# Kernel optimization log

Hardware: AMD Instinct MI355X
Metric: run time of the kernel (lower is better)

## Reference

```python
import jax, jax.numpy as jnp
import numpy as np

N_NODES = 100000
N_EDGES = 1600000
IN_FEAT = 128
OUT_FEAT = 64
RRELU_SLOPE = (1.0 / 8.0 + 1.0 / 3.0) / 2.0  # nn.RReLU eval-mode slope = 11/48


def setup_inputs() -> dict:
    key = jax.random.key(0)
    k1, k2, k3, k4, k5 = jax.random.split(key, 5)
    feat = jax.random.normal(k1, (N_NODES, IN_FEAT), dtype=jnp.float32)
    src = jax.random.randint(k2, (N_EDGES,), 0, N_NODES, dtype=jnp.int64)
    dst = jax.random.randint(k3, (N_EDGES,), 0, N_NODES, dtype=jnp.int64)
    # xavier-uniform-ish init
    b1 = np.sqrt(6.0 / (IN_FEAT + OUT_FEAT))
    b2 = np.sqrt(6.0 / (OUT_FEAT + OUT_FEAT))
    w1 = jax.random.uniform(k4, (IN_FEAT, OUT_FEAT), jnp.float32, -b1, b1)
    w2 = jax.random.uniform(k5, (OUT_FEAT, OUT_FEAT), jnp.float32, -b2, b2)
    return {"feat": feat, "src": src, "dst": dst, "w1": w1, "w2": w2}


def _gather_sum(h, src, dst):
    # DGL copy_src('h','m') + sum: for each dst node, sum messages from src nodes
    return jax.ops.segment_sum(h[src], dst, num_segments=N_NODES)


def _rrelu(x):
    return jnp.where(x >= 0, x, RRELU_SLOPE * x)


def reference(feat, src, dst, w1, w2):
    # pattern = 0: linear -> gather -> rrelu, linear -> gather -> rrelu
    h = feat @ w1                      # [N, out_feat]
    h = _gather_sum(h, src, dst)       # [N, out_feat]
    h = _rrelu(h)
    h = h @ w2                         # [N, out_feat]
    h = _gather_sum(h, src, dst)       # [N, out_feat]
    h = _rrelu(h)
    return h
```

## Files before the change

kernel.cpp:

```cpp
#include <hip/hip_runtime.h>

#define N_NODES 100000
#define N_EDGES 1600000
#define IN_FEAT 128
#define OUT_FEAT 64
#define SLOPE 0.22916666666666666f

#define NPB 128
#define NB 782
#define CAP 2560
#define BIN_CHUNK 8192
#define EPT 32
#define BIN_BLOCKS ((N_EDGES + BIN_CHUNK - 1) / BIN_CHUNK)
#define GEMM1_BLOCKS (N_NODES / 16)

__device__ __forceinline__ ushort f2bf(float x) {
    unsigned u = __float_as_uint(x);
    u += 0x7FFFu + ((u >> 16) & 1u);
    return (ushort)(u >> 16);
}

union FatSmem {
    struct { float f[16 * IN_FEAT]; float part[4 * 16 * OUT_FEAT]; } g;
    struct { int cnt[NB]; int gbase[NB]; } b;
};

__global__ __launch_bounds__(256) void gemm1_binning_kernel(
        const float* __restrict__ feat, const float* __restrict__ w1,
        ushort* __restrict__ h1,
        const int* __restrict__ src, const int* __restrict__ dst,
        int* __restrict__ bcur, int* __restrict__ pairs) {
    __shared__ FatSmem s;
    const int tid = threadIdx.x;

    if (blockIdx.x >= BIN_BLOCKS) {
        const int c = tid & 63;
        const int ks = tid >> 6;

        float wr[32];
#pragma unroll
        for (int j = 0; j < 32; ++j)
            wr[j] = w1[(ks * 32 + j) * OUT_FEAT + c];

        const int row0 = (blockIdx.x - BIN_BLOCKS) * 16;
        const float4* fg = (const float4*)(feat + (size_t)row0 * IN_FEAT);
        float4* fl = (float4*)s.g.f;
        fl[tid] = fg[tid];
        fl[tid + 256] = fg[tid + 256];
        __syncthreads();

        float acc[16];
#pragma unroll
        for (int r = 0; r < 16; ++r) acc[r] = 0.f;

        const float4* fv = (const float4*)s.g.f;
#pragma unroll
        for (int j4 = 0; j4 < 8; ++j4) {
            const float wa = wr[4 * j4], wb = wr[4 * j4 + 1];
            const float wc = wr[4 * j4 + 2], wd = wr[4 * j4 + 3];
#pragma unroll
            for (int r = 0; r < 16; ++r) {
                const float4 a = fv[r * 32 + ks * 8 + j4];
                acc[r] += a.x * wa + a.y * wb + a.z * wc + a.w * wd;
            }
        }

#pragma unroll
        for (int r = 0; r < 16; ++r)
            s.g.part[ks * (16 * OUT_FEAT) + r * OUT_FEAT + c] = acc[r];
        __syncthreads();

        ushort2* h1u2 = (ushort2*)h1;
#pragma unroll
        for (int half = 0; half < 2; ++half) {
            const int idx = half * 256 + tid;
            const int r = idx >> 5;
            const int cp = idx & 31;
            const float* p = s.g.part + r * OUT_FEAT + 2 * cp;
            const float lo = p[0] + p[1024] + p[2048] + p[3072];
            const float hi = p[1] + p[1025] + p[2049] + p[3073];
            h1u2[(size_t)(row0 + r) * 32 + cp] = make_ushort2(f2bf(lo), f2bf(hi));
        }
    } else {
        int* cnt = s.b.cnt;
        int* gbase = s.b.gbase;
        for (int i = tid; i < NB; i += 256) cnt[i] = 0;
        __syncthreads();
        const int base = blockIdx.x * BIN_CHUNK;
        int bl[EPT];
        int vp[EPT];
#pragma unroll
        for (int i = 0; i < EPT; ++i) {
            const int e = base + i * 256 + tid;
            if (e < N_EDGES) {
                const int d = dst[e];
                const int b = d >> 7;
                const int lpos = atomicAdd(&cnt[b], 1);
                bl[i] = (b << 13) | lpos;
                vp[i] = ((d & 127) << 17) | src[e];
            } else {
                bl[i] = -1;
            }
        }
        __syncthreads();
        for (int i = tid; i < NB; i += 256) {
            const int cc = cnt[i];
            gbase[i] = cc ? (i * CAP + atomicAdd(&bcur[i], cc)) : 0;
        }
        __syncthreads();
#pragma unroll
        for (int i = 0; i < EPT; ++i) {
            if (bl[i] >= 0) {
                const int b = bl[i] >> 13, lpos = bl[i] & 8191;
                pairs[gbase[b] + lpos] = vp[i];
            }
        }
    }
}

__global__ __launch_bounds__(256) void sort2_kernel(const int* __restrict__ pairs,
                                                    const int* __restrict__ bcur,
                                                    int* __restrict__ csr,
                                                    int2* __restrict__ nseg) {
    __shared__ int cnt[NPB];
    __shared__ int cur[NPB];
    __shared__ int wtot;
    const int b = blockIdx.x;
    const int t = threadIdx.x;
    const int beg = b * CAP;
    const int end = beg + bcur[b];
    if (t < NPB) cnt[t] = 0;
    __syncthreads();
    for (int i = beg + t; i < end; i += 256)
        atomicAdd(&cnt[pairs[i] >> 17], 1);
    __syncthreads();
    int v = 0, x = 0;
    const int lane = t & 63, w = t >> 6;
    if (t < NPB) {
        v = cnt[t];
        x = v;
#pragma unroll
        for (int off = 1; off < 64; off <<= 1) {
            int y = __shfl_up(x, off);
            if (lane >= off) x += y;
        }
        if (t == 63) wtot = x;
    }
    __syncthreads();
    if (t < NPB) {
        const int gp = beg + (x - v) + (w ? wtot : 0);
        cur[t] = gp;
        nseg[b * NPB + t] = make_int2(gp, gp + v);
    }
    __syncthreads();
    for (int i = beg + t; i < end; i += 256) {
        const int p = pairs[i];
        const int pos = atomicAdd(&cur[p >> 17], 1);
        csr[pos] = (p & 0x1FFFF) << 7;
    }
}

__device__ __forceinline__ float2 gather_pairs(const char* __restrict__ hb,
                                               const int* __restrict__ csr,
                                               int beg, int end, int hi, int cp4) {
    float ax = 0.f, ay = 0.f;
    int i = beg;
#define LOADU(k) const unsigned u##k = *(const unsigned*)(hb + (unsigned)(csr[i + 2*(k) + hi] + cp4))
#define ACCU(k)                                            \
    ax += __uint_as_float(u##k << 16);                     \
    ay += __uint_as_float(u##k & 0xFFFF0000u)
    for (; i + 16 <= end; i += 16) {
        LOADU(0); LOADU(1); LOADU(2); LOADU(3);
        LOADU(4); LOADU(5); LOADU(6); LOADU(7);
        ACCU(0); ACCU(1); ACCU(2); ACCU(3);
        ACCU(4); ACCU(5); ACCU(6); ACCU(7);
    }
    if (i + 8 <= end) {
        LOADU(0); LOADU(1); LOADU(2); LOADU(3);
        ACCU(0); ACCU(1); ACCU(2); ACCU(3);
        i += 8;
    }
    if (i + 4 <= end) {
        LOADU(0); LOADU(1);
        ACCU(0); ACCU(1);
        i += 4;
    }
    for (; i < end; i += 2) {
        if (i + hi < end) {
            const unsigned u = *(const unsigned*)(hb + (unsigned)(csr[i + hi] + cp4));
            ax += __uint_as_float(u << 16);
            ay += __uint_as_float(u & 0xFFFF0000u);
        }
    }
#undef LOADU
#undef ACCU
    return make_float2(ax, ay);
}

__global__ __launch_bounds__(256) void agg_gemm2_kernel(const ushort* __restrict__ h,
                                                        const int* __restrict__ csr,
                                                        const int2* __restrict__ nseg,
                                                        const float* __restrict__ w2,
                                                        ushort* __restrict__ h2) {
    __shared__ float w[OUT_FEAT * OUT_FEAT];
    __shared__ float rowbuf[4][OUT_FEAT];
    const int tid = threadIdx.x;

    const float4* w4g = (const float4*)w2;
    float4* wl = (float4*)w;
#pragma unroll
    for (int i = 0; i < 4; ++i) wl[tid + i * 256] = w4g[tid + i * 256];
    __syncthreads();

    const int wv = tid >> 6, c = tid & 63;
    const int hi = (tid >> 5) & 1, cp = tid & 31;
    const int node = blockIdx.x * 4 + wv;
    const int2 seg = nseg[node];
    const int beg = __builtin_amdgcn_readfirstlane(seg.x);
    const int end = __builtin_amdgcn_readfirstlane(seg.y);

    float2 acc = gather_pairs((const char*)h, csr, beg, end, hi, cp * 4);
    acc.x += __shfl_xor(acc.x, 32);
    acc.y += __shfl_xor(acc.y, 32);
    acc.x = acc.x >= 0.f ? acc.x : acc.x * SLOPE;
    acc.y = acc.y >= 0.f ? acc.y : acc.y * SLOPE;

    if (hi == 0) ((float2*)rowbuf[wv])[cp] = acc;

    float o = 0.f;
    const float4* rb4 = (const float4*)rowbuf[wv];
#pragma unroll
    for (int k = 0; k < OUT_FEAT; k += 4) {
        const float4 r = rb4[k >> 2];
        o += r.x * w[(k + 0) * OUT_FEAT + c] + r.y * w[(k + 1) * OUT_FEAT + c] +
             r.z * w[(k + 2) * OUT_FEAT + c] + r.w * w[(k + 3) * OUT_FEAT + c];
    }
    h2[(size_t)node * OUT_FEAT + c] = f2bf(o);
}

__global__ __launch_bounds__(256) void agg_rrelu_kernel(const ushort* __restrict__ h,
                                                        const int* __restrict__ csr,
                                                        const int2* __restrict__ nseg,
                                                        float* __restrict__ out) {
    const int tid = threadIdx.x;
    const int hi = (tid >> 5) & 1, cp = tid & 31;
    const int node = blockIdx.x * 4 + (tid >> 6);
    const int2 seg = nseg[node];
    const int beg = __builtin_amdgcn_readfirstlane(seg.x);
    const int end = __builtin_amdgcn_readfirstlane(seg.y);

    float2 acc = gather_pairs((const char*)h, csr, beg, end, hi, cp * 4);
    acc.x += __shfl_xor(acc.x, 32);
    acc.y += __shfl_xor(acc.y, 32);
    if (hi == 0) {
        acc.x = acc.x >= 0.f ? acc.x : acc.x * SLOPE;
        acc.y = acc.y >= 0.f ? acc.y : acc.y * SLOPE;
        ((float2*)(out + (size_t)node * OUT_FEAT))[cp] = acc;
    }
}

extern "C" void kernel_launch(void* const* d_in, const int* in_sizes, int n_in,
                              void* d_out, int out_size, void* d_ws, size_t ws_size,
                              hipStream_t stream) {
    const float* feat = (const float*)d_in[0];
    const int*   src  = (const int*)d_in[1];
    const int*   dst  = (const int*)d_in[2];
    const float* w1   = (const float*)d_in[3];
    const float* w2   = (const float*)d_in[4];
    float* out = (float*)d_out;

    ushort* h1   = (ushort*)d_ws;
    ushort* h2   = h1 + (size_t)N_NODES * OUT_FEAT;
    int*    pairs = (int*)h2;
    int*    csr  = (int*)(h2 + (size_t)N_NODES * OUT_FEAT);
    int2*   nseg = (int2*)(csr + NB * CAP);
    int*    bcur = (int*)(nseg + NB * NPB);

    hipMemsetAsync(bcur, 0, NB * sizeof(int), stream);
    gemm1_binning_kernel<<<BIN_BLOCKS + GEMM1_BLOCKS, 256, 0, stream>>>(
        feat, w1, h1, src, dst, bcur, pairs);
    sort2_kernel<<<NB, 256, 0, stream>>>(pairs, bcur, csr, nseg);

    agg_gemm2_kernel<<<N_NODES / 4, 256, 0, stream>>>(h1, csr, nseg, w2, h2);

    agg_rrelu_kernel<<<N_NODES / 4, 256, 0, stream>>>(h2, csr, nseg, out);
}
```

Baseline: 167.5 us.

## Widen gather to 8-byte quad loads and co-schedule GEMM1 with sort pass

The neighbor gather now has each 16-lane group load 4 bf16 features (8 bytes) per edge, processing 4 edges concurrently per wave. Edge indices are fetched with one coalesced csr read and broadcast by shuffles, followed by a cross-group reduction. Separately, the first GEMM moves from the binning launch to the sort launch, so binning runs alone and GEMM1 overlaps the per-bin counting sort. This aims to cut the number of gather memory instructions and rebalance work between launches, at the cost of extra shuffles and a reduction at the end.

```diff
diff --git a/kernel.cpp b/kernel.cpp
--- a/kernel.cpp
+++ b/kernel.cpp
@@ -20,20 +20,59 @@
     return (ushort)(u >> 16);
 }
 
-union FatSmem {
+__global__ __launch_bounds__(256) void binning_kernel(const int* __restrict__ src,
+                                                      const int* __restrict__ dst,
+                                                      int* __restrict__ bcur,
+                                                      int* __restrict__ pairs) {
+    __shared__ int cnt[NB];
+    __shared__ int gbase[NB];
+    for (int i = threadIdx.x; i < NB; i += 256) cnt[i] = 0;
+    __syncthreads();
+    const int base = blockIdx.x * BIN_CHUNK;
+    int bl[EPT];
+    int vp[EPT];
+#pragma unroll
+    for (int i = 0; i < EPT; ++i) {
+        const int e = base + i * 256 + threadIdx.x;
+        if (e < N_EDGES) {
+            const int d = dst[e];
+            const int b = d >> 7;
+            const int lpos = atomicAdd(&cnt[b], 1);
+            bl[i] = (b << 13) | lpos;
+            vp[i] = ((d & 127) << 17) | src[e];
+        } else {
+            bl[i] = -1;
+        }
+    }
+    __syncthreads();
+    for (int i = threadIdx.x; i < NB; i += 256) {
+        const int c = cnt[i];
+        gbase[i] = c ? (i * CAP + atomicAdd(&bcur[i], c)) : 0;
+    }
+    __syncthreads();
+#pragma unroll
+    for (int i = 0; i < EPT; ++i) {
+        if (bl[i] >= 0) {
+            const int b = bl[i] >> 13, lpos = bl[i] & 8191;
+            pairs[gbase[b] + lpos] = vp[i];
+        }
+    }
+}
+
+union Fat2Smem {
     struct { float f[16 * IN_FEAT]; float part[4 * 16 * OUT_FEAT]; } g;
-    struct { int cnt[NB]; int gbase[NB]; } b;
+    struct { int cnt[NPB]; int cur[NPB]; int wtot; } s;
 };
 
-__global__ __launch_bounds__(256) void gemm1_binning_kernel(
+__global__ __launch_bounds__(256) void sort2_gemm1_kernel(
+        const int* __restrict__ pairs, const int* __restrict__ bcur,
+        int* __restrict__ csr, int2* __restrict__ nseg,
         const float* __restrict__ feat, const float* __restrict__ w1,
-        ushort* __restrict__ h1,
-        const int* __restrict__ src, const int* __restrict__ dst,
-        int* __restrict__ bcur, int* __restrict__ pairs) {
-    __shared__ FatSmem s;
+        ushort* __restrict__ h1) {
+    __shared__ Fat2Smem u;
     const int tid = threadIdx.x;
 
-    if (blockIdx.x >= BIN_BLOCKS) {
+    if (blockIdx.x >= NB) {
         const int c = tid & 63;
         const int ks = tid >> 6;
 
@@ -42,9 +81,9 @@
         for (int j = 0; j < 32; ++j)
             wr[j] = w1[(ks * 32 + j) * OUT_FEAT + c];
 
-        const int row0 = (blockIdx.x - BIN_BLOCKS) * 16;
+        const int row0 = (blockIdx.x - NB) * 16;
         const float4* fg = (const float4*)(feat + (size_t)row0 * IN_FEAT);
-        float4* fl = (float4*)s.g.f;
+        float4* fl = (float4*)u.g.f;
         fl[tid] = fg[tid];
         fl[tid + 256] = fg[tid + 256];
         __syncthreads();
@@ -53,7 +92,7 @@
 #pragma unroll
         for (int r = 0; r < 16; ++r) acc[r] = 0.f;
 
-        const float4* fv = (const float4*)s.g.f;
+        const float4* fv = (const float4*)u.g.f;
 #pragma unroll
         for (int j4 = 0; j4 < 8; ++j4) {
             const float wa = wr[4 * j4], wb = wr[4 * j4 + 1];
@@ -67,7 +106,7 @@
 
 #pragma unroll
         for (int r = 0; r < 16; ++r)
-            s.g.part[ks * (16 * OUT_FEAT) + r * OUT_FEAT + c] = acc[r];
+            u.g.part[ks * (16 * OUT_FEAT) + r * OUT_FEAT + c] = acc[r];
         __syncthreads();
 
         ushort2* h1u2 = (ushort2*)h1;
@@ -76,125 +115,97 @@
             const int idx = half * 256 + tid;
             const int r = idx >> 5;
             const int cp = idx & 31;
-            const float* p = s.g.part + r * OUT_FEAT + 2 * cp;
+            const float* p = u.g.part + r * OUT_FEAT + 2 * cp;
             const float lo = p[0] + p[1024] + p[2048] + p[3072];
             const float hi = p[1] + p[1025] + p[2049] + p[3073];
             h1u2[(size_t)(row0 + r) * 32 + cp] = make_ushort2(f2bf(lo), f2bf(hi));
         }
     } else {
-        int* cnt = s.b.cnt;
-        int* gbase = s.b.gbase;
-        for (int i = tid; i < NB; i += 256) cnt[i] = 0;
-        __syncthreads();
-        const int base = blockIdx.x * BIN_CHUNK;
-        int bl[EPT];
-        int vp[EPT];
-#pragma unroll
-        for (int i = 0; i < EPT; ++i) {
-            const int e = base + i * 256 + tid;
-            if (e < N_EDGES) {
-                const int d = dst[e];
-                const int b = d >> 7;
-                const int lpos = atomicAdd(&cnt[b], 1);
-                bl[i] = (b << 13) | lpos;
-                vp[i] = ((d & 127) << 17) | src[e];
-            } else {
-                bl[i] = -1;
+        const int b = blockIdx.x;
+        const int beg = b * CAP;
+        const int end = beg + bcur[b];
+        if (tid < NPB) u.s.cnt[tid] = 0;
+        __syncthreads();
+        for (int i = beg + tid; i < end; i += 256)
+            atomicAdd(&u.s.cnt[pairs[i] >> 17], 1);
+        __syncthreads();
+        int v = 0, x = 0;
+        const int lane = tid & 63, w = tid >> 6;
+        if (tid < NPB) {
+            v = u.s.cnt[tid];
+            x = v;
+#pragma unroll
+            for (int off = 1; off < 64; off <<= 1) {
+                int y = __shfl_up(x, off);
+                if (lane >= off) x += y;
             }
-        }
-        __syncthreads();
-        for (int i = tid; i < NB; i += 256) {
-            const int cc = cnt[i];
-            gbase[i] = cc ? (i * CAP + atomicAdd(&bcur[i], cc)) : 0;
-        }
-        __syncthreads();
-#pragma unroll
-        for (int i = 0; i < EPT; ++i) {
-            if (bl[i] >= 0) {
-                const int b = bl[i] >> 13, lpos = bl[i] & 8191;
-                pairs[gbase[b] + lpos] = vp[i];
-            }
-        }
-    }
-}
-
-__global__ __launch_bounds__(256) void sort2_kernel(const int* __restrict__ pairs,
-                                                    const int* __restrict__ bcur,
-                                                    int* __restrict__ csr,
-                                                    int2* __restrict__ nseg) {
-    __shared__ int cnt[NPB];
-    __shared__ int cur[NPB];
-    __shared__ int wtot;
-    const int b = blockIdx.x;
-    const int t = threadIdx.x;
-    const int beg = b * CAP;
-    const int end = beg + bcur[b];
-    if (t < NPB) cnt[t] = 0;
-    __syncthreads();
-    for (int i = beg + t; i < end; i += 256)
-        atomicAdd(&cnt[pairs[i] >> 17], 1);
-    __syncthreads();
-    int v = 0, x = 0;
-    const int lane = t & 63, w = t >> 6;
-    if (t < NPB) {
-        v = cnt[t];
-        x = v;
-#pragma unroll
-        for (int off = 1; off < 64; off <<= 1) {
-            int y = __shfl_up(x, off);
-            if (lane >= off) x += y;
-        }
-        if (t == 63) wtot = x;
-    }
-    __syncthreads();
-    if (t < NPB) {
-        const int gp = beg + (x - v) + (w ? wtot : 0);
-        cur[t] = gp;
-        nseg[b * NPB + t] = make_int2(gp, gp + v);
-    }
-    __syncthreads();
-    for (int i = beg + t; i < end; i += 256) {
-        const int p = pairs[i];
-        const int pos = atomicAdd(&cur[p >> 17], 1);
-        csr[pos] = (p & 0x1FFFF) << 7;
-    }
-}
-
-__device__ __forceinline__ float2 gather_pairs(const char* __restrict__ hb,
-                                               const int* __restrict__ csr,
-                                               int beg, int end, int hi, int cp4) {
-    float ax = 0.f, ay = 0.f;
+            if (tid == 63) u.s.wtot = x;
+        }
+        __syncthreads();
+        if (tid < NPB) {
+            const int gp = beg + (x - v) + (w ? u.s.wtot : 0);
+            u.s.cur[tid] = gp;
+            nseg[b * NPB + tid] = make_int2(gp, gp + v);
+        }
+        __syncthreads();
+        for (int i = beg + tid; i < end; i += 256) {
+            const int p = pairs[i];
+            const int pos = atomicAdd(&u.s.cur[p >> 17], 1);
+            csr[pos] = (p & 0x1FFFF) << 7;
+        }
+    }
+}
+
+__device__ __forceinline__ float4 gather_quad(const char* __restrict__ hb,
+                                              const int* __restrict__ csr,
+                                              int beg, int end, int lane) {
+    const int g = (lane >> 4) & 3;
+    const unsigned q8 = (unsigned)((lane & 15) * 8);
+    float ax = 0.f, ay = 0.f, az = 0.f, aw = 0.f;
     int i = beg;
-#define LOADU(k) const unsigned u##k = *(const unsigned*)(hb + (unsigned)(csr[i + 2*(k) + hi] + cp4))
-#define ACCU(k)                                            \
-    ax += __uint_as_float(u##k << 16);                     \
-    ay += __uint_as_float(u##k & 0xFFFF0000u)
+#define QACC(u)                                   \
+    ax += __uint_as_float((u).x << 16);           \
+    ay += __uint_as_float((u).x & 0xFFFF0000u);   \
+    az += __uint_as_float((u).y << 16);           \
+    aw += __uint_as_float((u).y & 0xFFFF0000u)
     for (; i + 16 <= end; i += 16) {
-        LOADU(0); LOADU(1); LOADU(2); LOADU(3);
-        LOADU(4); LOADU(5); LOADU(6); LOADU(7);
-        ACCU(0); ACCU(1); ACCU(2); ACCU(3);
-        ACCU(4); ACCU(5); ACCU(6); ACCU(7);
-    }
-    if (i + 8 <= end) {
-        LOADU(0); LOADU(1); LOADU(2); LOADU(3);
-        ACCU(0); ACCU(1); ACCU(2); ACCU(3);
-        i += 8;
-    }
-    if (i + 4 <= end) {
-        LOADU(0); LOADU(1);
-        ACCU(0); ACCU(1);
-        i += 4;
-    }
-    for (; i < end; i += 2) {
-        if (i + hi < end) {
-            const unsigned u = *(const unsigned*)(hb + (unsigned)(csr[i + hi] + cp4));
-            ax += __uint_as_float(u << 16);
-            ay += __uint_as_float(u & 0xFFFF0000u);
-        }
-    }
-#undef LOADU
-#undef ACCU
-    return make_float2(ax, ay);
+        const int csv = csr[i + (lane & 15)];
+        const int r0 = __shfl(csv, g);
+        const int r1 = __shfl(csv, 4 + g);
+        const int r2 = __shfl(csv, 8 + g);
+        const int r3 = __shfl(csv, 12 + g);
+        const uint2 u0 = *(const uint2*)(hb + ((unsigned)r0 + q8));
+        const uint2 u1 = *(const uint2*)(hb + ((unsigned)r1 + q8));
+        const uint2 u2 = *(const uint2*)(hb + ((unsigned)r2 + q8));
+        const uint2 u3 = *(const uint2*)(hb + ((unsigned)r3 + q8));
+        QACC(u0); QACC(u1); QACC(u2); QACC(u3);
+    }
+    for (; i + 4 <= end; i += 4) {
+        const int c0 = csr[i], c1 = csr[i + 1], c2 = csr[i + 2], c3 = csr[i + 3];
+        const int r = g == 0 ? c0 : (g == 1 ? c1 : (g == 2 ? c2 : c3));
+        const uint2 u = *(const uint2*)(hb + ((unsigned)r + q8));
+        QACC(u);
+    }
+    if (i < end) {
+        const int rem = end - i;
+        const int r = csr[i + (g < rem ? g : 0)];
+        const uint2 u = *(const uint2*)(hb + ((unsigned)r + q8));
+        if (g < rem) { QACC(u); }
+    }
+#undef QACC
+    ax += __shfl_xor(ax, 16); ax += __shfl_xor(ax, 32);
+    ay += __shfl_xor(ay, 16); ay += __shfl_xor(ay, 32);
+    az += __shfl_xor(az, 16); az += __shfl_xor(az, 32);
+    aw += __shfl_xor(aw, 16); aw += __shfl_xor(aw, 32);
+    return make_float4(ax, ay, az, aw);
+}
+
+__device__ __forceinline__ float4 rrelu4(float4 v) {
+    v.x = v.x >= 0.f ? v.x : v.x * SLOPE;
+    v.y = v.y >= 0.f ? v.y : v.y * SLOPE;
+    v.z = v.z >= 0.f ? v.z : v.z * SLOPE;
+    v.w = v.w >= 0.f ? v.w : v.w * SLOPE;
+    return v;
 }
 
 __global__ __launch_bounds__(256) void agg_gemm2_kernel(const ushort* __restrict__ h,
@@ -212,20 +223,16 @@
     for (int i = 0; i < 4; ++i) wl[tid + i * 256] = w4g[tid + i * 256];
     __syncthreads();
 
-    const int wv = tid >> 6, c = tid & 63;
-    const int hi = (tid >> 5) & 1, cp = tid & 31;
+    const int wv = tid >> 6, lane = tid & 63, c = tid & 63;
     const int node = blockIdx.x * 4 + wv;
     const int2 seg = nseg[node];
     const int beg = __builtin_amdgcn_readfirstlane(seg.x);
     const int end = __builtin_amdgcn_readfirstlane(seg.y);
 
-    float2 acc = gather_pairs((const char*)h, csr, beg, end, hi, cp * 4);
-    acc.x += __shfl_xor(acc.x, 32);
-    acc.y += __shfl_xor(acc.y, 32);
-    acc.x = acc.x >= 0.f ? acc.x : acc.x * SLOPE;
-    acc.y = acc.y >= 0.f ? acc.y : acc.y * SLOPE;
-
-    if (hi == 0) ((float2*)rowbuf[wv])[cp] = acc;
+    float4 a = gather_quad((const char*)h, csr, beg, end, lane);
+    a = rrelu4(a);
+
+    if ((lane >> 4) == 0) ((float4*)rowbuf[wv])[lane & 15] = a;
 
     float o = 0.f;
     const float4* rb4 = (const float4*)rowbuf[wv];
@@ -243,19 +250,16 @@
                                                         const int2* __restrict__ nseg,
                                                         float* __restrict__ out) {
     const int tid = threadIdx.x;
-    const int hi = (tid >> 5) & 1, cp = tid & 31;
+    const int lane = tid & 63;
     const int node = blockIdx.x * 4 + (tid >> 6);
     const int2 seg = nseg[node];
     const int beg = __builtin_amdgcn_readfirstlane(seg.x);
     const int end = __builtin_amdgcn_readfirstlane(seg.y);
 
-    float2 acc = gather_pairs((const char*)h, csr, beg, end, hi, cp * 4);
-    acc.x += __shfl_xor(acc.x, 32);
-    acc.y += __shfl_xor(acc.y, 32);
-    if (hi == 0) {
-        acc.x = acc.x >= 0.f ? acc.x : acc.x * SLOPE;
-        acc.y = acc.y >= 0.f ? acc.y : acc.y * SLOPE;
-        ((float2*)(out + (size_t)node * OUT_FEAT))[cp] = acc;
+    float4 a = gather_quad((const char*)h, csr, beg, end, lane);
+    if ((lane >> 4) == 0) {
+        a = rrelu4(a);
+        ((float4*)(out + (size_t)node * OUT_FEAT))[lane & 15] = a;
     }
 }
 
@@ -277,9 +281,9 @@
     int*    bcur = (int*)(nseg + NB * NPB);
 
     hipMemsetAsync(bcur, 0, NB * sizeof(int), stream);
-    gemm1_binning_kernel<<<BIN_BLOCKS + GEMM1_BLOCKS, 256, 0, stream>>>(
-        feat, w1, h1, src, dst, bcur, pairs);
-    sort2_kernel<<<NB, 256, 0, stream>>>(pairs, bcur, csr, nseg);
+    binning_kernel<<<BIN_BLOCKS, 256, 0, stream>>>(src, dst, bcur, pairs);
+    sort2_gemm1_kernel<<<NB + GEMM1_BLOCKS, 256, 0, stream>>>(
+        pairs, bcur, csr, nseg, feat, w1, h1);
 
     agg_gemm2_kernel<<<N_NODES / 4, 256, 0, stream>>>(h1, csr, nseg, w2, h2);
 
```

After: 189.8 us (median of 2 runs). 1.13x slower.

## Pair gemm1 with sort stage instead of binning; transpose w2 in LDS

Applied to the files above, without the earlier changes.

Moves the feature GEMM blocks out of the binning launch and into the per-bucket sort launch, so the binning kernel runs alone and the sort work overlaps with the GEMM instead. In the aggregate+GEMM2 kernel, w2 is stored transposed in shared memory with padded rows, so each thread reads contiguous float4 weights rather than strided scalars. The rebalanced kernel split may change how well memory-bound binning and compute-bound GEMM overlap. The transposed store adds a strided global read of w2 per block.

```diff
diff --git a/kernel.cpp b/kernel.cpp
--- a/kernel.cpp
+++ b/kernel.cpp
@@ -13,6 +13,7 @@
 #define EPT 32
 #define BIN_BLOCKS ((N_EDGES + BIN_CHUNK - 1) / BIN_CHUNK)
 #define GEMM1_BLOCKS (N_NODES / 16)
+#define WTS 68
 
 __device__ __forceinline__ ushort f2bf(float x) {
     unsigned u = __float_as_uint(x);
@@ -20,20 +21,59 @@
     return (ushort)(u >> 16);
 }
 
-union FatSmem {
+__global__ __launch_bounds__(256) void binning_kernel(const int* __restrict__ src,
+                                                      const int* __restrict__ dst,
+                                                      int* __restrict__ bcur,
+                                                      int* __restrict__ pairs) {
+    __shared__ int cnt[NB];
+    __shared__ int gbase[NB];
+    for (int i = threadIdx.x; i < NB; i += 256) cnt[i] = 0;
+    __syncthreads();
+    const int base = blockIdx.x * BIN_CHUNK;
+    int bl[EPT];
+    int vp[EPT];
+#pragma unroll
+    for (int i = 0; i < EPT; ++i) {
+        const int e = base + i * 256 + threadIdx.x;
+        if (e < N_EDGES) {
+            const int d = dst[e];
+            const int b = d >> 7;
+            const int lpos = atomicAdd(&cnt[b], 1);
+            bl[i] = (b << 13) | lpos;
+            vp[i] = ((d & 127) << 17) | src[e];
+        } else {
+            bl[i] = -1;
+        }
+    }
+    __syncthreads();
+    for (int i = threadIdx.x; i < NB; i += 256) {
+        const int c = cnt[i];
+        gbase[i] = c ? (i * CAP + atomicAdd(&bcur[i], c)) : 0;
+    }
+    __syncthreads();
+#pragma unroll
+    for (int i = 0; i < EPT; ++i) {
+        if (bl[i] >= 0) {
+            const int b = bl[i] >> 13, lpos = bl[i] & 8191;
+            pairs[gbase[b] + lpos] = vp[i];
+        }
+    }
+}
+
+union Fat2Smem {
     struct { float f[16 * IN_FEAT]; float part[4 * 16 * OUT_FEAT]; } g;
-    struct { int cnt[NB]; int gbase[NB]; } b;
+    struct { int cnt[NPB]; int cur[NPB]; int wtot; } s;
 };
 
-__global__ __launch_bounds__(256) void gemm1_binning_kernel(
+__global__ __launch_bounds__(256) void sort2_gemm1_kernel(
+        const int* __restrict__ pairs, const int* __restrict__ bcur,
+        int* __restrict__ csr, int2* __restrict__ nseg,
         const float* __restrict__ feat, const float* __restrict__ w1,
-        ushort* __restrict__ h1,
-        const int* __restrict__ src, const int* __restrict__ dst,
-        int* __restrict__ bcur, int* __restrict__ pairs) {
-    __shared__ FatSmem s;
+        ushort* __restrict__ h1) {
+    __shared__ Fat2Smem u;
     const int tid = threadIdx.x;
 
-    if (blockIdx.x >= BIN_BLOCKS) {
+    if (blockIdx.x >= NB) {
         const int c = tid & 63;
         const int ks = tid >> 6;
 
@@ -42,9 +82,9 @@
         for (int j = 0; j < 32; ++j)
             wr[j] = w1[(ks * 32 + j) * OUT_FEAT + c];
 
-        const int row0 = (blockIdx.x - BIN_BLOCKS) * 16;
+        const int row0 = (blockIdx.x - NB) * 16;
         const float4* fg = (const float4*)(feat + (size_t)row0 * IN_FEAT);
-        float4* fl = (float4*)s.g.f;
+        float4* fl = (float4*)u.g.f;
         fl[tid] = fg[tid];
         fl[tid + 256] = fg[tid + 256];
         __syncthreads();
@@ -53,7 +93,7 @@
 #pragma unroll
         for (int r = 0; r < 16; ++r) acc[r] = 0.f;
 
-        const float4* fv = (const float4*)s.g.f;
+        const float4* fv = (const float4*)u.g.f;
 #pragma unroll
         for (int j4 = 0; j4 < 8; ++j4) {
             const float wa = wr[4 * j4], wb = wr[4 * j4 + 1];
@@ -67,7 +107,7 @@
 
 #pragma unroll
         for (int r = 0; r < 16; ++r)
-            s.g.part[ks * (16 * OUT_FEAT) + r * OUT_FEAT + c] = acc[r];
+            u.g.part[ks * (16 * OUT_FEAT) + r * OUT_FEAT + c] = acc[r];
         __syncthreads();
 
         ushort2* h1u2 = (ushort2*)h1;
@@ -76,87 +116,44 @@
             const int idx = half * 256 + tid;
             const int r = idx >> 5;
             const int cp = idx & 31;
-            const float* p = s.g.part + r * OUT_FEAT + 2 * cp;
+            const float* p = u.g.part + r * OUT_FEAT + 2 * cp;
             const float lo = p[0] + p[1024] + p[2048] + p[3072];
             const float hi = p[1] + p[1025] + p[2049] + p[3073];
             h1u2[(size_t)(row0 + r) * 32 + cp] = make_ushort2(f2bf(lo), f2bf(hi));
         }
     } else {
-        int* cnt = s.b.cnt;
-        int* gbase = s.b.gbase;
-        for (int i = tid; i < NB; i += 256) cnt[i] = 0;
-        __syncthreads();
-        const int base = blockIdx.x * BIN_CHUNK;
-        int bl[EPT];
-        int vp[EPT];
-#pragma unroll
-        for (int i = 0; i < EPT; ++i) {
-            const int e = base + i * 256 + tid;
-            if (e < N_EDGES) {
-                const int d = dst[e];
-                const int b = d >> 7;
-                const int lpos = atomicAdd(&cnt[b], 1);
-                bl[i] = (b << 13) | lpos;
-                vp[i] = ((d & 127) << 17) | src[e];
-            } else {
-                bl[i] = -1;
+        const int b = blockIdx.x;
+        const int beg = b * CAP;
+        const int end = beg + bcur[b];
+        if (tid < NPB) u.s.cnt[tid] = 0;
+        __syncthreads();
+        for (int i = beg + tid; i < end; i += 256)
+            atomicAdd(&u.s.cnt[pairs[i] >> 17], 1);
+        __syncthreads();
+        int v = 0, x = 0;
+        const int lane = tid & 63, w = tid >> 6;
+        if (tid < NPB) {
+            v = u.s.cnt[tid];
+            x = v;
+#pragma unroll
+            for (int off = 1; off < 64; off <<= 1) {
+                int y = __shfl_up(x, off);
+                if (lane >= off) x += y;
             }
-        }
-        __syncthreads();
-        for (int i = tid; i < NB; i += 256) {
-            const int cc = cnt[i];
-            gbase[i] = cc ? (i * CAP + atomicAdd(&bcur[i], cc)) : 0;
-        }
-        __syncthreads();
-#pragma unroll
-        for (int i = 0; i < EPT; ++i) {
-            if (bl[i] >= 0) {
-                const int b = bl[i] >> 13, lpos = bl[i] & 8191;
-                pairs[gbase[b] + lpos] = vp[i];
-            }
-        }
-    }
-}
-
-__global__ __launch_bounds__(256) void sort2_kernel(const int* __restrict__ pairs,
-                                                    const int* __restrict__ bcur,
-                                                    int* __restrict__ csr,
-                                                    int2* __restrict__ nseg) {
-    __shared__ int cnt[NPB];
-    __shared__ int cur[NPB];
-    __shared__ int wtot;
-    const int b = blockIdx.x;
-    const int t = threadIdx.x;
-    const int beg = b * CAP;
-    const int end = beg + bcur[b];
-    if (t < NPB) cnt[t] = 0;
-    __syncthreads();
-    for (int i = beg + t; i < end; i += 256)
-        atomicAdd(&cnt[pairs[i] >> 17], 1);
-    __syncthreads();
-    int v = 0, x = 0;
-    const int lane = t & 63, w = t >> 6;
-    if (t < NPB) {
-        v = cnt[t];
-        x = v;
-#pragma unroll
-        for (int off = 1; off < 64; off <<= 1) {
-            int y = __shfl_up(x, off);
-            if (lane >= off) x += y;
-        }
-        if (t == 63) wtot = x;
-    }
-    __syncthreads();
-    if (t < NPB) {
-        const int gp = beg + (x - v) + (w ? wtot : 0);
-        cur[t] = gp;
-        nseg[b * NPB + t] = make_int2(gp, gp + v);
-    }
-    __syncthreads();
-    for (int i = beg + t; i < end; i += 256) {
-        const int p = pairs[i];
-        const int pos = atomicAdd(&cur[p >> 17], 1);
-        csr[pos] = (p & 0x1FFFF) << 7;
+            if (tid == 63) u.s.wtot = x;
+        }
+        __syncthreads();
+        if (tid < NPB) {
+            const int gp = beg + (x - v) + (w ? u.s.wtot : 0);
+            u.s.cur[tid] = gp;
+            nseg[b * NPB + tid] = make_int2(gp, gp + v);
+        }
+        __syncthreads();
+        for (int i = beg + tid; i < end; i += 256) {
+            const int p = pairs[i];
+            const int pos = atomicAdd(&u.s.cur[p >> 17], 1);
+            csr[pos] = (p & 0x1FFFF) << 7;
+        }
     }
 }
 
@@ -202,17 +199,22 @@
                                                         const int2* __restrict__ nseg,
                                                         const float* __restrict__ w2,
                                                         ushort* __restrict__ h2) {
-    __shared__ float w[OUT_FEAT * OUT_FEAT];
+    __shared__ float wt[OUT_FEAT * WTS];
     __shared__ float rowbuf[4][OUT_FEAT];
     const int tid = threadIdx.x;
-
-    const float4* w4g = (const float4*)w2;
-    float4* wl = (float4*)w;
-#pragma unroll
-    for (int i = 0; i < 4; ++i) wl[tid + i * 256] = w4g[tid + i * 256];
-    __syncthreads();
-
-    const int wv = tid >> 6, c = tid & 63;
+    const int c = tid & 63;
+
+    {
+        const int kb = tid >> 6;
+#pragma unroll
+        for (int j = 0; j < 16; ++j) {
+            const int k = kb * 16 + j;
+            wt[c * WTS + k] = w2[k * OUT_FEAT + c];
+        }
+    }
+    __syncthreads();
+
+    const int wv = tid >> 6;
     const int hi = (tid >> 5) & 1, cp = tid & 31;
     const int node = blockIdx.x * 4 + wv;
     const int2 seg = nseg[node];
@@ -229,11 +231,12 @@
 
     float o = 0.f;
     const float4* rb4 = (const float4*)rowbuf[wv];
-#pragma unroll
-    for (int k = 0; k < OUT_FEAT; k += 4) {
-        const float4 r = rb4[k >> 2];
-        o += r.x * w[(k + 0) * OUT_FEAT + c] + r.y * w[(k + 1) * OUT_FEAT + c] +
-             r.z * w[(k + 2) * OUT_FEAT + c] + r.w * w[(k + 3) * OUT_FEAT + c];
+    const float4* wt4 = (const float4*)(wt + c * WTS);
+#pragma unroll
+    for (int j4 = 0; j4 < 16; ++j4) {
+        const float4 r = rb4[j4];
+        const float4 v = wt4[j4];
+        o += r.x * v.x + r.y * v.y + r.z * v.z + r.w * v.w;
     }
     h2[(size_t)node * OUT_FEAT + c] = f2bf(o);
 }
@@ -277,9 +280,9 @@
     int*    bcur = (int*)(nseg + NB * NPB);
 
     hipMemsetAsync(bcur, 0, NB * sizeof(int), stream);
-    gemm1_binning_kernel<<<BIN_BLOCKS + GEMM1_BLOCKS, 256, 0, stream>>>(
-        feat, w1, h1, src, dst, bcur, pairs);
-    sort2_kernel<<<NB, 256, 0, stream>>>(pairs, bcur, csr, nseg);
+    binning_kernel<<<BIN_BLOCKS, 256, 0, stream>>>(src, dst, bcur, pairs);
+    sort2_gemm1_kernel<<<NB + GEMM1_BLOCKS, 256, 0, stream>>>(
+        pairs, bcur, csr, nseg, feat, w1, h1);
 
     agg_gemm2_kernel<<<N_NODES / 4, 256, 0, stream>>>(h1, csr, nseg, w2, h2);
 
```

New measurement: 178.1 us, median of 2. +6.3%, slower.
